# Performance work log

Hardware: AMD Instinct MI355X
Metric: run time of the kernel (lower is better)

The kernel has to match this reference:

```python
import jax, jax.numpy as jnp
import numpy as np

B, SQ, SKV, D, H = 2, 2048, 2048, 1024, 16
HD = D // H  # 64
SIGMOID_BIAS = -8.0
LN_EPS = 1e-5


def setup_inputs() -> dict:
    key = jax.random.key(0)
    ks = jax.random.split(key, 6)
    s = D ** -0.5
    return {
        "q": jax.random.normal(ks[0], (B, SQ, D), dtype=jnp.float32),
        "kv": jax.random.normal(ks[1], (B, SKV, D), dtype=jnp.float32),
        "Wq": jax.random.normal(ks[2], (D, D), dtype=jnp.float32) * s,
        "Wkv": jax.random.normal(ks[3], (D, 2 * D), dtype=jnp.float32) * s,
        "v_gamma": jnp.ones((HD,), dtype=jnp.float32),
        "v_beta": jnp.zeros((HD,), dtype=jnp.float32),
        "Wproj": jax.random.normal(ks[4], (D, D), dtype=jnp.float32) * s,
    }


def _layernorm(x, gamma, beta):
    # LayerNorm over the last dim (head_dim)
    mu = jnp.mean(x, axis=-1, keepdims=True)
    var = jnp.mean(jnp.square(x - mu), axis=-1, keepdims=True)
    return (x - mu) * jax.lax.rsqrt(var + LN_EPS) * gamma + beta


def reference(q, kv, Wq, Wkv, v_gamma, v_beta, Wproj):
    # Projections (no bias)
    qh = (q @ Wq).reshape(B, SQ, H, HD)                    # [B,Sq,H,hd]
    kvh = (kv @ Wkv).reshape(B, SKV, 2, H, HD)
    k = kvh[:, :, 0]                                       # [B,Skv,H,hd]
    v = kvh[:, :, 1]
    # v_norm is always applied (qk_norm=False -> q/k norms are identity)
    v = _layernorm(v, v_gamma, v_beta)
    # prescale: scale both q and k by head_dim ** -0.25
    scale = HD ** -0.25
    logits = jnp.einsum("bqhd,bkhd->bhqk", qh * scale, k * scale)
    # sigmoid attention (no softmax normalization), causal mask:
    # score masked where i + Skv - Sq - j < 0  <=>  j > i (equal lengths)
    iq = jnp.arange(SQ)[:, None]
    jk = jnp.arange(SKV)[None, :]
    causal_mask = (jk <= iq + (SKV - SQ)).astype(logits.dtype)  # [Sq,Skv]
    attn = jax.nn.sigmoid(logits + SIGMOID_BIAS) * causal_mask
    attn_times_v = jnp.einsum("bhqk,bkhd->bqhd", attn, v).reshape(B, SQ, D)
    attn_proj = attn_times_v @ Wproj
    return attn_times_v, attn_proj
```

## Files before the change

kernel.cpp:

```cpp
#include <hip/hip_runtime.h>
#include <hip/hip_bf16.h>

#define B_ 2
#define SQ_ 2048
#define SKV_ 2048
#define D_ 1024
#define H_ 16
#define HD_ 64

typedef unsigned short u16;
typedef float f32x4 __attribute__((ext_vector_type(4)));
typedef float f32x16 __attribute__((ext_vector_type(16)));
typedef short s16x8 __attribute__((ext_vector_type(8)));

__device__ __forceinline__ u16 f2bf(float f) {
  union { float f; unsigned u; } v; v.f = f;
  return (u16)((v.u + 0x7FFFu + ((v.u >> 16) & 1u)) >> 16);
}
__device__ __forceinline__ float bf2f(u16 h) {
  union { unsigned u; float f; } v; v.u = ((unsigned)h) << 16;
  return v.f;
}
__device__ __forceinline__ unsigned pack2bf(float s0, float s1) {
  union { float f; unsigned u; } a, b; a.f = s0; b.f = s1;
  return __builtin_amdgcn_perm(b.u + 0x8000u, a.u + 0x8000u, 0x07060302u);
}
__device__ __forceinline__ f32x4 mfma16(s16x8 a, s16x8 b, f32x4 c) {
  return __builtin_amdgcn_mfma_f32_16x16x32_bf16(a, b, c, 0, 0, 0);
}
__device__ __forceinline__ f32x16 mfma32(s16x8 a, s16x8 b, f32x16 c) {
  return __builtin_amdgcn_mfma_f32_32x32x16_bf16(a, b, c, 0, 0, 0);
}
__device__ __forceinline__ void async16(const u16* g, u16* l) {
  __builtin_amdgcn_global_load_lds(
      (const __attribute__((address_space(1))) unsigned int*)g,
      (__attribute__((address_space(3))) unsigned int*)l, 16, 0, 0);
}

__device__ __forceinline__ void tr_tile(const float* __restrict__ in, u16* __restrict__ out,
                                        int R, int C, int cx, int ry, int t) {
  __shared__ u16 tile[32][33];
  int tx = t & 31, ty = t >> 5;
  int c0 = cx * 32, r0 = ry * 32;
#pragma unroll
  for (int i = 0; i < 4; i++)
    tile[ty + i * 8][tx] = f2bf(in[(size_t)(r0 + ty + i * 8) * C + c0 + tx]);
  __syncthreads();
#pragma unroll
  for (int i = 0; i < 4; i++)
    out[(size_t)(c0 + ty + i * 8) * R + r0 + tx] = tile[tx][ty + i * 8];
}

__device__ __forceinline__ void cast4(const float* __restrict__ in, u16* __restrict__ out,
                                      int i) {
  float4 f = *(const float4*)(in + i);
  ushort4 o;
  o.x = f2bf(f.x); o.y = f2bf(f.y); o.z = f2bf(f.z); o.w = f2bf(f.w);
  *(ushort4*)(out + i) = o;
}

__global__ __launch_bounds__(256) void prep_kernel(
    const float* __restrict__ q, u16* __restrict__ q_bf,
    const float* __restrict__ kv, u16* __restrict__ kv_bf,
    const float* __restrict__ Wq, u16* __restrict__ WqT,
    const float* __restrict__ Wkv, u16* __restrict__ WkvT,
    const float* __restrict__ Wproj, u16* __restrict__ WprT) {
  int bid = blockIdx.x, t = threadIdx.x;
  if (bid < 4096) {
    cast4(q, q_bf, bid * 1024 + t * 4);
  } else if (bid < 8192) {
    cast4(kv, kv_bf, (bid - 4096) * 1024 + t * 4);
  } else if (bid < 9216) {
    int b2 = bid - 8192;
    tr_tile(Wq, WqT, 1024, 1024, b2 & 31, b2 >> 5, t);
  } else if (bid < 11264) {
    int b2 = bid - 9216;
    tr_tile(Wkv, WkvT, 1024, 2048, b2 & 63, b2 >> 6, t);
  } else {
    int b2 = bid - 11264;
    tr_tile(Wproj, WprT, 1024, 1024, b2 & 31, b2 >> 5, t);
  }
}

template <int BM, int BN, bool OUT_BF16>
__device__ __forceinline__ void gemm_body(const u16* __restrict__ A,
                                          const u16* __restrict__ BT,
                                          void* __restrict__ Cout,
                                          int m0, int n0, int N, int K) {
  __shared__ __attribute__((aligned(16))) u16 As[BM][32];
  __shared__ __attribute__((aligned(16))) u16 Bs[BN][32];
  constexpr int AM = BM / 32, AN = BN / 32;
  int t = threadIdx.x, w = t >> 6, lane = t & 63;
  int l16 = lane & 15, quad = lane >> 4;
  int mw = (w >> 1) * (BM / 2), nw = (w & 1) * (BN / 2);
  int grow = w * 16 + (lane >> 2);
  int gcol = (lane & 3) * 8;

  f32x4 acc[AM][AN] = {};

  for (int kt = 0; kt < K; kt += 32) {
    __syncthreads();
#pragma unroll
    for (int j = 0; j < BM / 64; j++)
      async16(A + (size_t)(m0 + j * 64 + grow) * K + kt + gcol, &As[j * 64 + w * 16][0]);
#pragma unroll
    for (int j = 0; j < BN / 64; j++)
      async16(BT + (size_t)(n0 + j * 64 + grow) * K + kt + gcol, &Bs[j * 64 + w * 16][0]);
    __syncthreads();
    s16x8 af[AM], bf[AN];
#pragma unroll
    for (int i = 0; i < AM; i++) af[i] = *(const s16x8*)&As[mw + i * 16 + l16][quad * 8];
#pragma unroll
    for (int j = 0; j < AN; j++) bf[j] = *(const s16x8*)&Bs[nw + j * 16 + l16][quad * 8];
#pragma unroll
    for (int i = 0; i < AM; i++)
#pragma unroll
      for (int j = 0; j < AN; j++)
        acc[i][j] = mfma16(af[i], bf[j], acc[i][j]);
  }

#pragma unroll
  for (int i = 0; i < AM; i++)
#pragma unroll
    for (int j = 0; j < AN; j++) {
      int col = n0 + nw + j * 16 + l16;
#pragma unroll
      for (int r = 0; r < 4; r++) {
        int row = m0 + mw + i * 16 + quad * 4 + r;
        float v = acc[i][j][r];
        if (OUT_BF16)
          ((u16*)Cout)[(size_t)row * N + col] = f2bf(v);
        else
          ((float*)Cout)[(size_t)row * N + col] = v;
      }
    }
}

__global__ __launch_bounds__(256, 3) void gemm_qkv(const u16* __restrict__ q_bf,
                                                   const u16* __restrict__ WqT,
                                                   u16* __restrict__ qh,
                                                   const u16* __restrict__ kv_bf,
                                                   const u16* __restrict__ WkvT,
                                                   u16* __restrict__ kvh) {
  int bx = blockIdx.x;
  if (bx < 8)
    gemm_body<128, 128, true>(q_bf, WqT, qh, blockIdx.y * 128, bx * 128, D_, D_);
  else
    gemm_body<128, 128, true>(kv_bf, WkvT, kvh, blockIdx.y * 128, (bx - 8) * 128, 2 * D_, D_);
}

__global__ __launch_bounds__(256, 3) void gemm_proj(const u16* __restrict__ A,
                                                    const u16* __restrict__ BT,
                                                    float* __restrict__ C) {
  gemm_body<64, 128, false>(A, BT, C, blockIdx.y * 64, blockIdx.x * 128, D_, D_);
}

__global__ __launch_bounds__(256) void ln_vt_kernel(const u16* __restrict__ kvh,
                                                    const float* __restrict__ gamma,
                                                    const float* __restrict__ beta,
                                                    u16* __restrict__ vt) {
  __shared__ __attribute__((aligned(16))) u16 tile[64][72];
  int bid = blockIdx.x;
  int stile = bid & 31;
  int h = (bid >> 5) & 15;
  int b = bid >> 9;
  int wave = threadIdx.x >> 6, lane = threadIdx.x & 63;
  float g = gamma[lane], be = beta[lane];
#pragma unroll 4
  for (int i = 0; i < 16; i++) {
    int s = stile * 64 + wave * 16 + i;
    float x = bf2f(kvh[(size_t)(b * SKV_ + s) * 2048 + 1024 + h * 64 + lane]);
    float sum = x;
#pragma unroll
    for (int off = 32; off; off >>= 1) sum += __shfl_xor(sum, off, 64);
    float mu = sum * (1.0f / 64.0f);
    float dx = x - mu;
    float s2 = dx * dx;
#pragma unroll
    for (int off = 32; off; off >>= 1) s2 += __shfl_xor(s2, off, 64);
    float inv = rsqrtf(s2 * (1.0f / 64.0f) + 1e-5f);
    tile[lane][wave * 16 + i] = f2bf(dx * inv * g + be);
  }
  __syncthreads();
  int d = threadIdx.x >> 2, sc = (threadIdx.x & 3) * 16;
  size_t orow = ((size_t)(b * H_ + h) * 64 + d) * SKV_ + stile * 64 + sc;
  uint4 v0 = *(const uint4*)&tile[d][sc];
  uint4 v1 = *(const uint4*)&tile[d][sc + 8];
  *(uint4*)(vt + orow) = v0;
  *(uint4*)(vt + orow + 8) = v1;
}

__global__ __launch_bounds__(256, 4) void attn_kernel(const u16* __restrict__ qh,
                                                      const u16* __restrict__ kvh,
                                                      const u16* __restrict__ vt,
                                                      float* __restrict__ out0,
                                                      u16* __restrict__ atv_bf) {
  __shared__ __attribute__((aligned(16))) u16 Ks[2][64][68];
  __shared__ __attribute__((aligned(16))) u16 Vs[2][64][68];

  int bh = blockIdx.x;
  int qt = 31 - blockIdx.y;
  int h = bh & 15, b = bh >> 4;
  int t = threadIdx.x;
  int w = t >> 6, lane = t & 63;
  int l31 = lane & 31, hi = lane >> 5;
  int qs = w & 1, kh = w >> 1;
  int srow = t >> 2;
  int scol = (t & 3) * 16;

  const float C1 = -0.18033688011f;
  const float C2 = 11.5415603272f;

  const u16* gkb = kvh + ((size_t)(b * SKV_) + srow) * 2048 + h * 64 + scol;
  const u16* gvb = vt + ((size_t)((b * H_ + h) * 64 + srow)) * 2048 + scol;
  float* Osc = (float*)&Ks[0][0][0];

  int q0 = qt * 64;
  int nkv = qt + 1;

  s16x8 qf[4];
  {
    const u16* qp = qh + (size_t)(b * SQ_ + q0 + qs * 32 + l31) * D_ + h * 64 + hi * 8;
#pragma unroll
    for (int c = 0; c < 4; c++) qf[c] = *(const s16x8*)(qp + c * 16);
  }

  f32x16 oacc[2] = {};

  uint4 kr0 = *(const uint4*)gkb, kr1 = *(const uint4*)(gkb + 8);
  uint4 vr0 = *(const uint4*)gvb, vr1 = *(const uint4*)(gvb + 8);

  for (int kt = 0; kt < nkv; kt++) {
    int buf = kt & 1;
    *(uint4*)&Ks[buf][srow][scol] = kr0; *(uint4*)&Ks[buf][srow][scol + 8] = kr1;
    *(uint4*)&Vs[buf][srow][scol] = vr0; *(uint4*)&Vs[buf][srow][scol + 8] = vr1;
    __syncthreads();
    if (kt + 1 < nkv) {
      const u16* gk2 = gkb + (size_t)(kt + 1) * 64 * 2048;
      const u16* gv2 = gvb + (size_t)(kt + 1) * 64;
      kr0 = *(const uint4*)gk2; kr1 = *(const uint4*)(gk2 + 8);
      vr0 = *(const uint4*)gv2; vr1 = *(const uint4*)(gv2 + 8);
    }

    f32x16 st = {};
#pragma unroll
    for (int c = 0; c < 4; c++) {
      s16x8 kf = *(const s16x8*)&Ks[buf][kh * 32 + l31][c * 16 + hi * 8];
      st = mfma32(kf, qf[c], st);
    }

    unsigned u[8];
    if (kt == nkv - 1) {
      int qi = q0 + qs * 32 + l31;
      int kbase = kt * 64 + kh * 32 + 4 * hi;
#pragma unroll
      for (int g = 0; g < 4; g++) {
        float pv4[4];
#pragma unroll
        for (int i = 0; i < 4; i++) {
          float s = st[4 * g + i];
          float e = __builtin_amdgcn_exp2f(s * C1 + C2);
          float p = __builtin_amdgcn_rcpf(1.0f + e);
          pv4[i] = (kbase + 8 * g + i > qi) ? 0.0f : p;
        }
        u[2 * g] = pack2bf(pv4[0], pv4[1]);
        u[2 * g + 1] = pack2bf(pv4[2], pv4[3]);
      }
    } else {
#pragma unroll
      for (int g = 0; g < 4; g++) {
        float pv4[4];
#pragma unroll
        for (int i = 0; i < 4; i++) {
          float s = st[4 * g + i];
          float e = __builtin_amdgcn_exp2f(s * C1 + C2);
          pv4[i] = __builtin_amdgcn_rcpf(1.0f + e);
        }
        u[2 * g] = pack2bf(pv4[0], pv4[1]);
        u[2 * g + 1] = pack2bf(pv4[2], pv4[3]);
      }
    }

    union { unsigned wd[4]; s16x8 v; } pa0, pa1;
    {
      auto r02 = __builtin_amdgcn_permlane32_swap(u[0], u[2], false, false);
      auto r13 = __builtin_amdgcn_permlane32_swap(u[1], u[3], false, false);
      auto r46 = __builtin_amdgcn_permlane32_swap(u[4], u[6], false, false);
      auto r57 = __builtin_amdgcn_permlane32_swap(u[5], u[7], false, false);
      pa0.wd[0] = r02[0]; pa0.wd[1] = r13[0]; pa0.wd[2] = r02[1]; pa0.wd[3] = r13[1];
      pa1.wd[0] = r46[0]; pa1.wd[1] = r57[0]; pa1.wd[2] = r46[1]; pa1.wd[3] = r57[1];
    }

#pragma unroll
    for (int dt = 0; dt < 2; dt++) {
      s16x8 vf0 = *(const s16x8*)&Vs[buf][dt * 32 + l31][kh * 32 + hi * 8];
      oacc[dt] = mfma32(pa0.v, vf0, oacc[dt]);
      s16x8 vf1 = *(const s16x8*)&Vs[buf][dt * 32 + l31][kh * 32 + 16 + hi * 8];
      oacc[dt] = mfma32(pa1.v, vf1, oacc[dt]);
    }
  }

  __syncthreads();
  if (kh == 1) {
#pragma unroll
    for (int dt = 0; dt < 2; dt++)
#pragma unroll
      for (int reg = 0; reg < 16; reg++) {
        int ql = (reg & 3) + 8 * (reg >> 2) + 4 * hi;
        Osc[(qs * 32 + ql) * 66 + dt * 32 + l31] = oacc[dt][reg];
      }
  }
  __syncthreads();
  if (kh == 0) {
#pragma unroll
    for (int dt = 0; dt < 2; dt++)
#pragma unroll
      for (int reg = 0; reg < 16; reg++) {
        int ql = (reg & 3) + 8 * (reg >> 2) + 4 * hi;
        float v = oacc[dt][reg] + Osc[(qs * 32 + ql) * 66 + dt * 32 + l31];
        int row = q0 + qs * 32 + ql;
        int col = h * 64 + dt * 32 + l31;
        size_t idx = (size_t)(b * SQ_ + row) * D_ + col;
        out0[idx] = v;
        atv_bf[idx] = f2bf(v);
      }
  }
}

extern "C" void kernel_launch(void* const* d_in, const int* in_sizes, int n_in,
                              void* d_out, int out_size, void* d_ws, size_t ws_size,
                              hipStream_t stream) {
  const float* q      = (const float*)d_in[0];
  const float* kv     = (const float*)d_in[1];
  const float* Wq     = (const float*)d_in[2];
  const float* Wkv    = (const float*)d_in[3];
  const float* vgamma = (const float*)d_in[4];
  const float* vbeta  = (const float*)d_in[5];
  const float* Wproj  = (const float*)d_in[6];
  float* out0 = (float*)d_out;
  float* out1 = out0 + (size_t)B_ * SQ_ * D_;

  char* p = (char*)d_ws;
  u16* q_bf  = (u16*)p; p += (size_t)B_ * SQ_ * D_ * 2;
  u16* kv_bf = (u16*)p; p += (size_t)B_ * SKV_ * D_ * 2;
  u16* WqT   = (u16*)p; p += (size_t)D_ * D_ * 2;
  u16* WkvT  = (u16*)p; p += (size_t)2 * D_ * D_ * 2;
  u16* WprT  = (u16*)p; p += (size_t)D_ * D_ * 2;
  u16* qh    = (u16*)p; p += (size_t)B_ * SQ_ * D_ * 2;
  u16* kvh   = (u16*)p; p += (size_t)B_ * SKV_ * 2 * D_ * 2;
  u16* vt    = (u16*)p; p += (size_t)B_ * H_ * HD_ * SKV_ * 2;
  u16* atv   = (u16*)p; p += (size_t)B_ * SQ_ * D_ * 2;

  prep_kernel<<<dim3(12288), 256, 0, stream>>>(q, q_bf, kv, kv_bf, Wq, WqT, Wkv, WkvT, Wproj, WprT);

  gemm_qkv<<<dim3(24, 32), 256, 0, stream>>>(q_bf, WqT, qh, kv_bf, WkvT, kvh);

  ln_vt_kernel<<<dim3((B_ * H_ * SKV_) / 64), 256, 0, stream>>>(kvh, vgamma, vbeta, vt);

  attn_kernel<<<dim3(32, 32), 256, 0, stream>>>(qh, kvh, vt, out0, atv);

  gemm_proj<<<dim3(8, 64), 256, 0, stream>>>(atv, WprT, out1);
}
```

Measured before the change: 200.9 us.

## Load K/V fragments directly from global memory and split KV tiles across waves

```diff
diff --git a/kernel.cpp b/kernel.cpp
--- a/kernel.cpp
+++ b/kernel.cpp
@@ -190,135 +190,104 @@
   *(uint4*)(vt + orow + 8) = v1;
 }
 
+template <bool MASKED>
+__device__ __forceinline__ void attn_tile(const u16* __restrict__ kb,
+                                          const u16* __restrict__ vb,
+                                          const s16x8* qf, f32x16* oacc,
+                                          int qi, int kbase) {
+  s16x8 vf0 = *(const s16x8*)(vb);
+  s16x8 vf1 = *(const s16x8*)(vb + 16);
+  s16x8 vf2 = *(const s16x8*)(vb + (size_t)32 * SKV_);
+  s16x8 vf3 = *(const s16x8*)(vb + (size_t)32 * SKV_ + 16);
+  f32x16 st = {};
+#pragma unroll
+  for (int c = 0; c < 4; c++) {
+    s16x8 kf = *(const s16x8*)(kb + c * 16);
+    st = mfma32(kf, qf[c], st);
+  }
+  const float C1 = -0.18033688011f;
+  const float C2 = 11.5415603272f;
+  unsigned u[8];
+#pragma unroll
+  for (int g = 0; g < 4; g++) {
+    float pv4[4];
+#pragma unroll
+    for (int i = 0; i < 4; i++) {
+      float s = st[4 * g + i];
+      float e = __builtin_amdgcn_exp2f(s * C1 + C2);
+      float p = __builtin_amdgcn_rcpf(1.0f + e);
+      pv4[i] = (MASKED && (kbase + 8 * g + i > qi)) ? 0.0f : p;
+    }
+    u[2 * g] = pack2bf(pv4[0], pv4[1]);
+    u[2 * g + 1] = pack2bf(pv4[2], pv4[3]);
+  }
+  union { unsigned wd[4]; s16x8 v; } pa0, pa1;
+  auto r02 = __builtin_amdgcn_permlane32_swap(u[0], u[2], false, false);
+  auto r13 = __builtin_amdgcn_permlane32_swap(u[1], u[3], false, false);
+  auto r46 = __builtin_amdgcn_permlane32_swap(u[4], u[6], false, false);
+  auto r57 = __builtin_amdgcn_permlane32_swap(u[5], u[7], false, false);
+  pa0.wd[0] = r02[0]; pa0.wd[1] = r13[0]; pa0.wd[2] = r02[1]; pa0.wd[3] = r13[1];
+  pa1.wd[0] = r46[0]; pa1.wd[1] = r57[0]; pa1.wd[2] = r46[1]; pa1.wd[3] = r57[1];
+  __builtin_amdgcn_s_setprio(1);
+  oacc[0] = mfma32(pa0.v, vf0, oacc[0]);
+  oacc[0] = mfma32(pa1.v, vf1, oacc[0]);
+  oacc[1] = mfma32(pa0.v, vf2, oacc[1]);
+  oacc[1] = mfma32(pa1.v, vf3, oacc[1]);
+  __builtin_amdgcn_s_setprio(0);
+}
+
 __global__ __launch_bounds__(256, 4) void attn_kernel(const u16* __restrict__ qh,
                                                       const u16* __restrict__ kvh,
                                                       const u16* __restrict__ vt,
                                                       float* __restrict__ out0,
                                                       u16* __restrict__ atv_bf) {
-  __shared__ __attribute__((aligned(16))) u16 Ks[2][64][68];
-  __shared__ __attribute__((aligned(16))) u16 Vs[2][64][68];
+  __shared__ __attribute__((aligned(16))) float Osc[2][32][66];
 
   int bh = blockIdx.x;
-  int qt = 31 - blockIdx.y;
+  int qb = 31 - blockIdx.y;
   int h = bh & 15, b = bh >> 4;
-  int t = threadIdx.x;
-  int w = t >> 6, lane = t & 63;
+  int t = threadIdx.x, w = t >> 6, lane = t & 63;
   int l31 = lane & 31, hi = lane >> 5;
-  int qs = w & 1, kh = w >> 1;
-  int srow = t >> 2;
-  int scol = (t & 3) * 16;
-
-  const float C1 = -0.18033688011f;
-  const float C2 = 11.5415603272f;
-
-  const u16* gkb = kvh + ((size_t)(b * SKV_) + srow) * 2048 + h * 64 + scol;
-  const u16* gvb = vt + ((size_t)((b * H_ + h) * 64 + srow)) * 2048 + scol;
-  float* Osc = (float*)&Ks[0][0][0];
-
-  int q0 = qt * 64;
-  int nkv = qt + 1;
+  int sl = w >> 1, r = w & 1;
+  int qrow0 = qb * 64 + sl * 32;
+  int s_tile = qrow0 >> 5;
+  int qi = qrow0 + l31;
 
   s16x8 qf[4];
   {
-    const u16* qp = qh + (size_t)(b * SQ_ + q0 + qs * 32 + l31) * D_ + h * 64 + hi * 8;
+    const u16* qp = qh + (size_t)(b * SQ_ + qrow0 + l31) * D_ + h * 64 + hi * 8;
 #pragma unroll
     for (int c = 0; c < 4; c++) qf[c] = *(const s16x8*)(qp + c * 16);
   }
+  const u16* kb0 = kvh + ((size_t)b * SKV_ + l31) * 2048 + h * 64 + hi * 8;
+  const u16* vb0 = vt + ((size_t)((b * H_ + h) * 64) + l31) * SKV_ + hi * 8;
 
   f32x16 oacc[2] = {};
 
-  uint4 kr0 = *(const uint4*)gkb, kr1 = *(const uint4*)(gkb + 8);
-  uint4 vr0 = *(const uint4*)gvb, vr1 = *(const uint4*)(gvb + 8);
-
-  for (int kt = 0; kt < nkv; kt++) {
-    int buf = kt & 1;
-    *(uint4*)&Ks[buf][srow][scol] = kr0; *(uint4*)&Ks[buf][srow][scol + 8] = kr1;
-    *(uint4*)&Vs[buf][srow][scol] = vr0; *(uint4*)&Vs[buf][srow][scol + 8] = vr1;
-    __syncthreads();
-    if (kt + 1 < nkv) {
-      const u16* gk2 = gkb + (size_t)(kt + 1) * 64 * 2048;
-      const u16* gv2 = gvb + (size_t)(kt + 1) * 64;
-      kr0 = *(const uint4*)gk2; kr1 = *(const uint4*)(gk2 + 8);
-      vr0 = *(const uint4*)gv2; vr1 = *(const uint4*)(gv2 + 8);
-    }
-
-    f32x16 st = {};
-#pragma unroll
-    for (int c = 0; c < 4; c++) {
-      s16x8 kf = *(const s16x8*)&Ks[buf][kh * 32 + l31][c * 16 + hi * 8];
-      st = mfma32(kf, qf[c], st);
-    }
-
-    unsigned u[8];
-    if (kt == nkv - 1) {
-      int qi = q0 + qs * 32 + l31;
-      int kbase = kt * 64 + kh * 32 + 4 * hi;
-#pragma unroll
-      for (int g = 0; g < 4; g++) {
-        float pv4[4];
-#pragma unroll
-        for (int i = 0; i < 4; i++) {
-          float s = st[4 * g + i];
-          float e = __builtin_amdgcn_exp2f(s * C1 + C2);
-          float p = __builtin_amdgcn_rcpf(1.0f + e);
-          pv4[i] = (kbase + 8 * g + i > qi) ? 0.0f : p;
-        }
-        u[2 * g] = pack2bf(pv4[0], pv4[1]);
-        u[2 * g + 1] = pack2bf(pv4[2], pv4[3]);
-      }
-    } else {
-#pragma unroll
-      for (int g = 0; g < 4; g++) {
-        float pv4[4];
-#pragma unroll
-        for (int i = 0; i < 4; i++) {
-          float s = st[4 * g + i];
-          float e = __builtin_amdgcn_exp2f(s * C1 + C2);
-          pv4[i] = __builtin_amdgcn_rcpf(1.0f + e);
-        }
-        u[2 * g] = pack2bf(pv4[0], pv4[1]);
-        u[2 * g + 1] = pack2bf(pv4[2], pv4[3]);
-      }
-    }
-
-    union { unsigned wd[4]; s16x8 v; } pa0, pa1;
-    {
-      auto r02 = __builtin_amdgcn_permlane32_swap(u[0], u[2], false, false);
-      auto r13 = __builtin_amdgcn_permlane32_swap(u[1], u[3], false, false);
-      auto r46 = __builtin_amdgcn_permlane32_swap(u[4], u[6], false, false);
-      auto r57 = __builtin_amdgcn_permlane32_swap(u[5], u[7], false, false);
-      pa0.wd[0] = r02[0]; pa0.wd[1] = r13[0]; pa0.wd[2] = r02[1]; pa0.wd[3] = r13[1];
-      pa1.wd[0] = r46[0]; pa1.wd[1] = r57[0]; pa1.wd[2] = r46[1]; pa1.wd[3] = r57[1];
-    }
-
-#pragma unroll
-    for (int dt = 0; dt < 2; dt++) {
-      s16x8 vf0 = *(const s16x8*)&Vs[buf][dt * 32 + l31][kh * 32 + hi * 8];
-      oacc[dt] = mfma32(pa0.v, vf0, oacc[dt]);
-      s16x8 vf1 = *(const s16x8*)&Vs[buf][dt * 32 + l31][kh * 32 + 16 + hi * 8];
-      oacc[dt] = mfma32(pa1.v, vf1, oacc[dt]);
-    }
-  }
-
-  __syncthreads();
-  if (kh == 1) {
+  for (int kt = r; kt < s_tile; kt += 2)
+    attn_tile<false>(kb0 + (size_t)kt * 32 * 2048, vb0 + kt * 32, qf, oacc, 0, 0);
+  if ((s_tile & 1) == r)
+    attn_tile<true>(kb0 + (size_t)s_tile * 32 * 2048, vb0 + s_tile * 32, qf, oacc,
+                    qi, s_tile * 32 + 4 * hi);
+
+  if (r == 1) {
 #pragma unroll
     for (int dt = 0; dt < 2; dt++)
 #pragma unroll
       for (int reg = 0; reg < 16; reg++) {
         int ql = (reg & 3) + 8 * (reg >> 2) + 4 * hi;
-        Osc[(qs * 32 + ql) * 66 + dt * 32 + l31] = oacc[dt][reg];
+        Osc[sl][ql][dt * 32 + l31] = oacc[dt][reg];
       }
   }
   __syncthreads();
-  if (kh == 0) {
+  if (r == 0) {
 #pragma unroll
     for (int dt = 0; dt < 2; dt++)
 #pragma unroll
       for (int reg = 0; reg < 16; reg++) {
         int ql = (reg & 3) + 8 * (reg >> 2) + 4 * hi;
-        float v = oacc[dt][reg] + Osc[(qs * 32 + ql) * 66 + dt * 32 + l31];
-        int row = q0 + qs * 32 + ql;
+        float v = oacc[dt][reg] + Osc[sl][ql][dt * 32 + l31];
+        int row = qrow0 + ql;
         int col = h * 64 + dt * 32 + l31;
         size_t idx = (size_t)(b * SQ_ + row) * D_ + col;
         out0[idx] = v;
```

After: 241.3 us. +20.1%, slower.

## Restructure attention to 128-row Q tiles with per-wave full KV rows

Applied to the files above, without the earlier changes.

```diff
diff --git a/kernel.cpp b/kernel.cpp
--- a/kernel.cpp
+++ b/kernel.cpp
@@ -190,7 +190,74 @@
   *(uint4*)(vt + orow + 8) = v1;
 }
 
-__global__ __launch_bounds__(256, 4) void attn_kernel(const u16* __restrict__ qh,
+template <bool MASKED>
+__device__ __forceinline__ void attn_compute(const u16* __restrict__ Kb,
+                                             const u16* __restrict__ Vb,
+                                             const s16x8* qf, f32x16* oacc,
+                                             int qi, int kt, int l31, int hi) {
+  f32x16 st0 = {}, st1 = {};
+  __builtin_amdgcn_s_setprio(1);
+#pragma unroll
+  for (int c = 0; c < 4; c++) {
+    s16x8 kf0 = *(const s16x8*)(Kb + (size_t)l31 * 68 + c * 16 + hi * 8);
+    s16x8 kf1 = *(const s16x8*)(Kb + (size_t)(32 + l31) * 68 + c * 16 + hi * 8);
+    st0 = mfma32(kf0, qf[c], st0);
+    st1 = mfma32(kf1, qf[c], st1);
+  }
+  __builtin_amdgcn_s_setprio(0);
+
+  const float C1 = -0.18033688011f;
+  const float C2 = 11.5415603272f;
+  unsigned u0[8], u1[8];
+  int kb0 = kt * 64 + 4 * hi;
+  int kb1 = kt * 64 + 32 + 4 * hi;
+#pragma unroll
+  for (int g = 0; g < 4; g++) {
+    float a4[4], b4[4];
+#pragma unroll
+    for (int i = 0; i < 4; i++) {
+      float e0 = __builtin_amdgcn_exp2f(st0[4 * g + i] * C1 + C2);
+      float p0 = __builtin_amdgcn_rcpf(1.0f + e0);
+      a4[i] = (MASKED && (kb0 + 8 * g + i > qi)) ? 0.0f : p0;
+      float e1 = __builtin_amdgcn_exp2f(st1[4 * g + i] * C1 + C2);
+      float p1 = __builtin_amdgcn_rcpf(1.0f + e1);
+      b4[i] = (MASKED && (kb1 + 8 * g + i > qi)) ? 0.0f : p1;
+    }
+    u0[2 * g] = pack2bf(a4[0], a4[1]); u0[2 * g + 1] = pack2bf(a4[2], a4[3]);
+    u1[2 * g] = pack2bf(b4[0], b4[1]); u1[2 * g + 1] = pack2bf(b4[2], b4[3]);
+  }
+
+  union { unsigned wd[4]; s16x8 v; } pa[4];
+  {
+    auto r02 = __builtin_amdgcn_permlane32_swap(u0[0], u0[2], false, false);
+    auto r13 = __builtin_amdgcn_permlane32_swap(u0[1], u0[3], false, false);
+    auto r46 = __builtin_amdgcn_permlane32_swap(u0[4], u0[6], false, false);
+    auto r57 = __builtin_amdgcn_permlane32_swap(u0[5], u0[7], false, false);
+    pa[0].wd[0] = r02[0]; pa[0].wd[1] = r13[0]; pa[0].wd[2] = r02[1]; pa[0].wd[3] = r13[1];
+    pa[1].wd[0] = r46[0]; pa[1].wd[1] = r57[0]; pa[1].wd[2] = r46[1]; pa[1].wd[3] = r57[1];
+  }
+  {
+    auto r02 = __builtin_amdgcn_permlane32_swap(u1[0], u1[2], false, false);
+    auto r13 = __builtin_amdgcn_permlane32_swap(u1[1], u1[3], false, false);
+    auto r46 = __builtin_amdgcn_permlane32_swap(u1[4], u1[6], false, false);
+    auto r57 = __builtin_amdgcn_permlane32_swap(u1[5], u1[7], false, false);
+    pa[2].wd[0] = r02[0]; pa[2].wd[1] = r13[0]; pa[2].wd[2] = r02[1]; pa[2].wd[3] = r13[1];
+    pa[3].wd[0] = r46[0]; pa[3].wd[1] = r57[0]; pa[3].wd[2] = r46[1]; pa[3].wd[3] = r57[1];
+  }
+
+  __builtin_amdgcn_s_setprio(1);
+#pragma unroll
+  for (int dt = 0; dt < 2; dt++) {
+#pragma unroll
+    for (int kc = 0; kc < 4; kc++) {
+      s16x8 vf = *(const s16x8*)(Vb + (size_t)(dt * 32 + l31) * 68 + kc * 16 + hi * 8);
+      oacc[dt] = mfma32(pa[kc].v, vf, oacc[dt]);
+    }
+  }
+  __builtin_amdgcn_s_setprio(0);
+}
+
+__global__ __launch_bounds__(256, 3) void attn_kernel(const u16* __restrict__ qh,
                                                       const u16* __restrict__ kvh,
                                                       const u16* __restrict__ vt,
                                                       float* __restrict__ out0,
@@ -199,28 +266,24 @@
   __shared__ __attribute__((aligned(16))) u16 Vs[2][64][68];
 
   int bh = blockIdx.x;
-  int qt = 31 - blockIdx.y;
+  int qb = 15 - blockIdx.y;
   int h = bh & 15, b = bh >> 4;
-  int t = threadIdx.x;
-  int w = t >> 6, lane = t & 63;
+  int t = threadIdx.x, w = t >> 6, lane = t & 63;
   int l31 = lane & 31, hi = lane >> 5;
-  int qs = w & 1, kh = w >> 1;
   int srow = t >> 2;
   int scol = (t & 3) * 16;
 
-  const float C1 = -0.18033688011f;
-  const float C2 = 11.5415603272f;
+  int qrow0 = qb * 128 + w * 32;
+  int qi = qrow0 + l31;
+  int mydiag = 2 * qb + (w >> 1);
+  int nkv = 2 * qb + 2;
 
   const u16* gkb = kvh + ((size_t)(b * SKV_) + srow) * 2048 + h * 64 + scol;
   const u16* gvb = vt + ((size_t)((b * H_ + h) * 64 + srow)) * 2048 + scol;
-  float* Osc = (float*)&Ks[0][0][0];
-
-  int q0 = qt * 64;
-  int nkv = qt + 1;
 
   s16x8 qf[4];
   {
-    const u16* qp = qh + (size_t)(b * SQ_ + q0 + qs * 32 + l31) * D_ + h * 64 + hi * 8;
+    const u16* qp = qh + (size_t)(b * SQ_ + qi) * D_ + h * 64 + hi * 8;
 #pragma unroll
     for (int c = 0; c < 4; c++) qf[c] = *(const s16x8*)(qp + c * 16);
   }
@@ -241,90 +304,24 @@
       kr0 = *(const uint4*)gk2; kr1 = *(const uint4*)(gk2 + 8);
       vr0 = *(const uint4*)gv2; vr1 = *(const uint4*)(gv2 + 8);
     }
-
-    f32x16 st = {};
-#pragma unroll
-    for (int c = 0; c < 4; c++) {
-      s16x8 kf = *(const s16x8*)&Ks[buf][kh * 32 + l31][c * 16 + hi * 8];
-      st = mfma32(kf, qf[c], st);
-    }
-
-    unsigned u[8];
-    if (kt == nkv - 1) {
-      int qi = q0 + qs * 32 + l31;
-      int kbase = kt * 64 + kh * 32 + 4 * hi;
-#pragma unroll
-      for (int g = 0; g < 4; g++) {
-        float pv4[4];
-#pragma unroll
-        for (int i = 0; i < 4; i++) {
-          float s = st[4 * g + i];
-          float e = __builtin_amdgcn_exp2f(s * C1 + C2);
-          float p = __builtin_amdgcn_rcpf(1.0f + e);
-          pv4[i] = (kbase + 8 * g + i > qi) ? 0.0f : p;
-        }
-        u[2 * g] = pack2bf(pv4[0], pv4[1]);
-        u[2 * g + 1] = pack2bf(pv4[2], pv4[3]);
-      }
-    } else {
-#pragma unroll
-      for (int g = 0; g < 4; g++) {
-        float pv4[4];
-#pragma unroll
-        for (int i = 0; i < 4; i++) {
-          float s = st[4 * g + i];
-          float e = __builtin_amdgcn_exp2f(s * C1 + C2);
-          pv4[i] = __builtin_amdgcn_rcpf(1.0f + e);
-        }
-        u[2 * g] = pack2bf(pv4[0], pv4[1]);
-        u[2 * g + 1] = pack2bf(pv4[2], pv4[3]);
-      }
-    }
-
-    union { unsigned wd[4]; s16x8 v; } pa0, pa1;
-    {
-      auto r02 = __builtin_amdgcn_permlane32_swap(u[0], u[2], false, false);
-      auto r13 = __builtin_amdgcn_permlane32_swap(u[1], u[3], false, false);
-      auto r46 = __builtin_amdgcn_permlane32_swap(u[4], u[6], false, false);
-      auto r57 = __builtin_amdgcn_permlane32_swap(u[5], u[7], false, false);
-      pa0.wd[0] = r02[0]; pa0.wd[1] = r13[0]; pa0.wd[2] = r02[1]; pa0.wd[3] = r13[1];
-      pa1.wd[0] = r46[0]; pa1.wd[1] = r57[0]; pa1.wd[2] = r46[1]; pa1.wd[3] = r57[1];
-    }
-
-#pragma unroll
-    for (int dt = 0; dt < 2; dt++) {
-      s16x8 vf0 = *(const s16x8*)&Vs[buf][dt * 32 + l31][kh * 32 + hi * 8];
-      oacc[dt] = mfma32(pa0.v, vf0, oacc[dt]);
-      s16x8 vf1 = *(const s16x8*)&Vs[buf][dt * 32 + l31][kh * 32 + 16 + hi * 8];
-      oacc[dt] = mfma32(pa1.v, vf1, oacc[dt]);
-    }
-  }
-
-  __syncthreads();
-  if (kh == 1) {
-#pragma unroll
-    for (int dt = 0; dt < 2; dt++)
-#pragma unroll
-      for (int reg = 0; reg < 16; reg++) {
-        int ql = (reg & 3) + 8 * (reg >> 2) + 4 * hi;
-        Osc[(qs * 32 + ql) * 66 + dt * 32 + l31] = oacc[dt][reg];
-      }
-  }
-  __syncthreads();
-  if (kh == 0) {
-#pragma unroll
-    for (int dt = 0; dt < 2; dt++)
-#pragma unroll
-      for (int reg = 0; reg < 16; reg++) {
-        int ql = (reg & 3) + 8 * (reg >> 2) + 4 * hi;
-        float v = oacc[dt][reg] + Osc[(qs * 32 + ql) * 66 + dt * 32 + l31];
-        int row = q0 + qs * 32 + ql;
-        int col = h * 64 + dt * 32 + l31;
-        size_t idx = (size_t)(b * SQ_ + row) * D_ + col;
-        out0[idx] = v;
-        atv_bf[idx] = f2bf(v);
-      }
-  }
+    if (kt < mydiag)
+      attn_compute<false>(&Ks[buf][0][0], &Vs[buf][0][0], qf, oacc, qi, kt, l31, hi);
+    else if (kt == mydiag)
+      attn_compute<true>(&Ks[buf][0][0], &Vs[buf][0][0], qf, oacc, qi, kt, l31, hi);
+  }
+
+#pragma unroll
+  for (int dt = 0; dt < 2; dt++)
+#pragma unroll
+    for (int reg = 0; reg < 16; reg++) {
+      int ql = (reg & 3) + 8 * (reg >> 2) + 4 * hi;
+      float v = oacc[dt][reg];
+      int row = qrow0 + ql;
+      int col = h * 64 + dt * 32 + l31;
+      size_t idx = (size_t)(b * SQ_ + row) * D_ + col;
+      out0[idx] = v;
+      atv_bf[idx] = f2bf(v);
+    }
 }
 
 extern "C" void kernel_launch(void* const* d_in, const int* in_sizes, int n_in,
@@ -357,7 +354,7 @@
 
   ln_vt_kernel<<<dim3((B_ * H_ * SKV_) / 64), 256, 0, stream>>>(kvh, vgamma, vbeta, vt);
 
-  attn_kernel<<<dim3(32, 32), 256, 0, stream>>>(qh, kvh, vt, out0, atv);
+  attn_kernel<<<dim3(32, 16), 256, 0, stream>>>(qh, kvh, vt, out0, atv);
 
   gemm_proj<<<dim3(8, 64), 256, 0, stream>>>(atv, WprT, out1);
 }
```

After: 263.4 us. 1.31x slower.

## Fuse V LayerNorm and transpose into the KV projection GEMM epilogue

Applied to the files above, without the earlier changes.

```diff
diff --git a/kernel.cpp b/kernel.cpp
--- a/kernel.cpp
+++ b/kernel.cpp
@@ -82,13 +82,17 @@
   }
 }
 
-template <int BM, int BN, bool OUT_BF16>
+template <int BM, int BN, bool OUT_BF16, bool LNV>
 __device__ __forceinline__ void gemm_body(const u16* __restrict__ A,
                                           const u16* __restrict__ BT,
                                           void* __restrict__ Cout,
-                                          int m0, int n0, int N, int K) {
-  __shared__ __attribute__((aligned(16))) u16 As[BM][32];
-  __shared__ __attribute__((aligned(16))) u16 Bs[BN][32];
+                                          int m0, int n0, int N, int K,
+                                          u16* __restrict__ smem,
+                                          const float* __restrict__ gamma,
+                                          const float* __restrict__ beta,
+                                          u16* __restrict__ vt) {
+  u16* As = smem;
+  u16* Bs = smem + BM * 32;
   constexpr int AM = BM / 32, AN = BN / 32;
   int t = threadIdx.x, w = t >> 6, lane = t & 63;
   int l16 = lane & 15, quad = lane >> 4;
@@ -102,21 +106,74 @@
     __syncthreads();
 #pragma unroll
     for (int j = 0; j < BM / 64; j++)
-      async16(A + (size_t)(m0 + j * 64 + grow) * K + kt + gcol, &As[j * 64 + w * 16][0]);
+      async16(A + (size_t)(m0 + j * 64 + grow) * K + kt + gcol, &As[(j * 64 + w * 16) * 32]);
 #pragma unroll
     for (int j = 0; j < BN / 64; j++)
-      async16(BT + (size_t)(n0 + j * 64 + grow) * K + kt + gcol, &Bs[j * 64 + w * 16][0]);
+      async16(BT + (size_t)(n0 + j * 64 + grow) * K + kt + gcol, &Bs[(j * 64 + w * 16) * 32]);
     __syncthreads();
     s16x8 af[AM], bf[AN];
 #pragma unroll
-    for (int i = 0; i < AM; i++) af[i] = *(const s16x8*)&As[mw + i * 16 + l16][quad * 8];
-#pragma unroll
-    for (int j = 0; j < AN; j++) bf[j] = *(const s16x8*)&Bs[nw + j * 16 + l16][quad * 8];
+    for (int i = 0; i < AM; i++) af[i] = *(const s16x8*)&As[(mw + i * 16 + l16) * 32 + quad * 8];
+#pragma unroll
+    for (int j = 0; j < AN; j++) bf[j] = *(const s16x8*)&Bs[(nw + j * 16 + l16) * 32 + quad * 8];
 #pragma unroll
     for (int i = 0; i < AM; i++)
 #pragma unroll
       for (int j = 0; j < AN; j++)
         acc[i][j] = mfma16(af[i], bf[j], acc[i][j]);
+  }
+
+  if constexpr (LNV) {
+    __syncthreads();
+    u16* tile = smem + w * 4352;
+    int h = (n0 - 1024 + nw) >> 6;
+    int b_ = m0 >> 11;
+    int s0 = (m0 & 2047) + mw;
+    float g4[4], be4[4];
+#pragma unroll
+    for (int j = 0; j < 4; j++) { g4[j] = gamma[j * 16 + l16]; be4[j] = beta[j * 16 + l16]; }
+#pragma unroll
+    for (int i = 0; i < 4; i++) {
+      float mu[4], inv[4];
+#pragma unroll
+      for (int r = 0; r < 4; r++) {
+        float x0 = acc[i][0][r], x1 = acc[i][1][r], x2 = acc[i][2][r], x3 = acc[i][3][r];
+        float rs = x0 + x1 + x2 + x3;
+        rs += __shfl_xor(rs, 1); rs += __shfl_xor(rs, 2);
+        rs += __shfl_xor(rs, 4); rs += __shfl_xor(rs, 8);
+        float m = rs * 0.015625f;
+        float d0 = x0 - m, d1 = x1 - m, d2 = x2 - m, d3 = x3 - m;
+        float vs = d0 * d0 + d1 * d1 + d2 * d2 + d3 * d3;
+        vs += __shfl_xor(vs, 1); vs += __shfl_xor(vs, 2);
+        vs += __shfl_xor(vs, 4); vs += __shfl_xor(vs, 8);
+        mu[r] = m;
+        inv[r] = rsqrtf(vs * 0.015625f + 1e-5f);
+      }
+#pragma unroll
+      for (int j = 0; j < 4; j++) {
+        ushort4 o;
+        o.x = f2bf((acc[i][j][0] - mu[0]) * inv[0] * g4[j] + be4[j]);
+        o.y = f2bf((acc[i][j][1] - mu[1]) * inv[1] * g4[j] + be4[j]);
+        o.z = f2bf((acc[i][j][2] - mu[2]) * inv[2] * g4[j] + be4[j]);
+        o.w = f2bf((acc[i][j][3] - mu[3]) * inv[3] * g4[j] + be4[j]);
+        *(ushort4*)&tile[(size_t)(j * 16 + l16) * 68 + i * 16 + quad * 4] = o;
+      }
+    }
+    size_t vbase = ((size_t)((b_ * 16 + h) * 64)) * 2048 + s0;
+#pragma unroll
+    for (int p = 0; p < 4; p++) {
+      int d = p * 16 + (lane >> 2);
+      int sc = (lane & 3) * 16;
+      uint2 a0 = *(uint2*)&tile[(size_t)d * 68 + sc];
+      uint2 a1 = *(uint2*)&tile[(size_t)d * 68 + sc + 4];
+      uint2 a2 = *(uint2*)&tile[(size_t)d * 68 + sc + 8];
+      uint2 a3 = *(uint2*)&tile[(size_t)d * 68 + sc + 12];
+      uint4 w0; w0.x = a0.x; w0.y = a0.y; w0.z = a1.x; w0.w = a1.y;
+      uint4 w1; w1.x = a2.x; w1.y = a2.y; w1.z = a3.x; w1.w = a3.y;
+      *(uint4*)(vt + vbase + (size_t)d * 2048 + sc) = w0;
+      *(uint4*)(vt + vbase + (size_t)d * 2048 + sc + 8) = w1;
+    }
+    return;
   }
 
 #pragma unroll
@@ -141,57 +198,34 @@
                                                    u16* __restrict__ qh,
                                                    const u16* __restrict__ kv_bf,
                                                    const u16* __restrict__ WkvT,
-                                                   u16* __restrict__ kvh) {
+                                                   u16* __restrict__ kh,
+                                                   const float* __restrict__ gamma,
+                                                   const float* __restrict__ beta,
+                                                   u16* __restrict__ vt) {
+  __shared__ __attribute__((aligned(16))) u16 smem[17408];
   int bx = blockIdx.x;
   if (bx < 8)
-    gemm_body<128, 128, true>(q_bf, WqT, qh, blockIdx.y * 128, bx * 128, D_, D_);
+    gemm_body<128, 128, true, false>(q_bf, WqT, qh, blockIdx.y * 128, bx * 128, D_, D_,
+                                     smem, nullptr, nullptr, nullptr);
+  else if (bx < 16)
+    gemm_body<128, 128, true, false>(kv_bf, WkvT, kh, blockIdx.y * 128, (bx - 8) * 128, D_, D_,
+                                     smem, nullptr, nullptr, nullptr);
   else
-    gemm_body<128, 128, true>(kv_bf, WkvT, kvh, blockIdx.y * 128, (bx - 8) * 128, 2 * D_, D_);
+    gemm_body<128, 128, true, true>(kv_bf, WkvT, nullptr, blockIdx.y * 128,
+                                    1024 + (bx - 16) * 128, 0, D_,
+                                    smem, gamma, beta, vt);
 }
 
 __global__ __launch_bounds__(256, 3) void gemm_proj(const u16* __restrict__ A,
                                                     const u16* __restrict__ BT,
                                                     float* __restrict__ C) {
-  gemm_body<64, 128, false>(A, BT, C, blockIdx.y * 64, blockIdx.x * 128, D_, D_);
-}
-
-__global__ __launch_bounds__(256) void ln_vt_kernel(const u16* __restrict__ kvh,
-                                                    const float* __restrict__ gamma,
-                                                    const float* __restrict__ beta,
-                                                    u16* __restrict__ vt) {
-  __shared__ __attribute__((aligned(16))) u16 tile[64][72];
-  int bid = blockIdx.x;
-  int stile = bid & 31;
-  int h = (bid >> 5) & 15;
-  int b = bid >> 9;
-  int wave = threadIdx.x >> 6, lane = threadIdx.x & 63;
-  float g = gamma[lane], be = beta[lane];
-#pragma unroll 4
-  for (int i = 0; i < 16; i++) {
-    int s = stile * 64 + wave * 16 + i;
-    float x = bf2f(kvh[(size_t)(b * SKV_ + s) * 2048 + 1024 + h * 64 + lane]);
-    float sum = x;
-#pragma unroll
-    for (int off = 32; off; off >>= 1) sum += __shfl_xor(sum, off, 64);
-    float mu = sum * (1.0f / 64.0f);
-    float dx = x - mu;
-    float s2 = dx * dx;
-#pragma unroll
-    for (int off = 32; off; off >>= 1) s2 += __shfl_xor(s2, off, 64);
-    float inv = rsqrtf(s2 * (1.0f / 64.0f) + 1e-5f);
-    tile[lane][wave * 16 + i] = f2bf(dx * inv * g + be);
-  }
-  __syncthreads();
-  int d = threadIdx.x >> 2, sc = (threadIdx.x & 3) * 16;
-  size_t orow = ((size_t)(b * H_ + h) * 64 + d) * SKV_ + stile * 64 + sc;
-  uint4 v0 = *(const uint4*)&tile[d][sc];
-  uint4 v1 = *(const uint4*)&tile[d][sc + 8];
-  *(uint4*)(vt + orow) = v0;
-  *(uint4*)(vt + orow + 8) = v1;
+  __shared__ __attribute__((aligned(16))) u16 smem[(64 + 128) * 32];
+  gemm_body<64, 128, false, false>(A, BT, C, blockIdx.y * 64, blockIdx.x * 128, D_, D_,
+                                   smem, nullptr, nullptr, nullptr);
 }
 
 __global__ __launch_bounds__(256, 4) void attn_kernel(const u16* __restrict__ qh,
-                                                      const u16* __restrict__ kvh,
+                                                      const u16* __restrict__ kh_buf,
                                                       const u16* __restrict__ vt,
                                                       float* __restrict__ out0,
                                                       u16* __restrict__ atv_bf) {
@@ -211,7 +245,7 @@
   const float C1 = -0.18033688011f;
   const float C2 = 11.5415603272f;
 
-  const u16* gkb = kvh + ((size_t)(b * SKV_) + srow) * 2048 + h * 64 + scol;
+  const u16* gkb = kh_buf + ((size_t)(b * SKV_) + srow) * 1024 + h * 64 + scol;
   const u16* gvb = vt + ((size_t)((b * H_ + h) * 64 + srow)) * 2048 + scol;
   float* Osc = (float*)&Ks[0][0][0];
 
@@ -236,7 +270,7 @@
     *(uint4*)&Vs[buf][srow][scol] = vr0; *(uint4*)&Vs[buf][srow][scol + 8] = vr1;
     __syncthreads();
     if (kt + 1 < nkv) {
-      const u16* gk2 = gkb + (size_t)(kt + 1) * 64 * 2048;
+      const u16* gk2 = gkb + (size_t)(kt + 1) * 64 * 1024;
       const u16* gv2 = gvb + (size_t)(kt + 1) * 64;
       kr0 = *(const uint4*)gk2; kr1 = *(const uint4*)(gk2 + 8);
       vr0 = *(const uint4*)gv2; vr1 = *(const uint4*)(gv2 + 8);
@@ -347,17 +381,15 @@
   u16* WkvT  = (u16*)p; p += (size_t)2 * D_ * D_ * 2;
   u16* WprT  = (u16*)p; p += (size_t)D_ * D_ * 2;
   u16* qh    = (u16*)p; p += (size_t)B_ * SQ_ * D_ * 2;
-  u16* kvh   = (u16*)p; p += (size_t)B_ * SKV_ * 2 * D_ * 2;
+  u16* kh    = (u16*)p; p += (size_t)B_ * SKV_ * D_ * 2;
   u16* vt    = (u16*)p; p += (size_t)B_ * H_ * HD_ * SKV_ * 2;
   u16* atv   = (u16*)p; p += (size_t)B_ * SQ_ * D_ * 2;
 
   prep_kernel<<<dim3(12288), 256, 0, stream>>>(q, q_bf, kv, kv_bf, Wq, WqT, Wkv, WkvT, Wproj, WprT);
 
-  gemm_qkv<<<dim3(24, 32), 256, 0, stream>>>(q_bf, WqT, qh, kv_bf, WkvT, kvh);
-
-  ln_vt_kernel<<<dim3((B_ * H_ * SKV_) / 64), 256, 0, stream>>>(kvh, vgamma, vbeta, vt);
-
-  attn_kernel<<<dim3(32, 32), 256, 0, stream>>>(qh, kvh, vt, out0, atv);
+  gemm_qkv<<<dim3(24, 32), 256, 0, stream>>>(q_bf, WqT, qh, kv_bf, WkvT, kh, vgamma, vbeta, vt);
+
+  attn_kernel<<<dim3(32, 32), 256, 0, stream>>>(qh, kh, vt, out0, atv);
 
   gemm_proj<<<dim3(8, 64), 256, 0, stream>>>(atv, WprT, out1);
 }
```

Result: faster. 190.1 us (-5.4%).
